# Kernel optimization log

Hardware: AMD Instinct MI355X
Metric: run time of the kernel (lower is better)

The kernel has to match this reference:

```python
import jax, jax.numpy as jnp
import numpy as np

N = 100_000   # nodes
E = 1_600_000 # edges
F = 128       # feature_dim
H = 128       # hidden_dim
C = 16        # num_classes


def setup_inputs() -> dict:
    key = jax.random.key(0)
    ks = jax.random.split(key, 7)
    x = jax.random.normal(ks[0], (N, F), dtype=jnp.float32)
    edge_index = jax.random.randint(ks[1], (2, E), 0, N, dtype=jnp.int64)
    edge_attr = jax.random.uniform(ks[2], (E,), dtype=jnp.float32)
    W1 = jax.random.normal(ks[3], (F, H), dtype=jnp.float32) / np.float32(np.sqrt(F))
    b1 = jnp.zeros((H,), jnp.float32)
    W2 = jax.random.normal(ks[4], (H, C), dtype=jnp.float32) / np.float32(np.sqrt(H))
    b2 = jnp.zeros((C,), jnp.float32)
    return {"x": x, "edge_index": edge_index, "edge_attr": edge_attr,
            "W1": W1, "b1": b1, "W2": W2, "b2": b2}


def gcn_conv(x, src, dst, ew, W, b, n):
    # PyG GCNConv: add self-loops (weight 1), symmetric degree normalization,
    # linear transform, weighted scatter-sum to destinations, bias after aggregation.
    loop = jnp.arange(n, dtype=src.dtype)
    s = jnp.concatenate([src, loop])
    d = jnp.concatenate([dst, loop])
    w = jnp.concatenate([ew, jnp.ones((n,), ew.dtype)])
    deg = jax.ops.segment_sum(w, d, num_segments=n)           # [N]
    dinv = jnp.where(deg > 0, jax.lax.rsqrt(deg), 0.0)
    norm = dinv[s] * w * dinv[d]                               # [E+N]
    h = x @ W                                                  # [N, out]
    out = jax.ops.segment_sum(h[s] * norm[:, None], d, num_segments=n)
    return out + b


def reference(x, edge_index, edge_attr, W1, b1, W2, b2):
    src, dst = edge_index[0], edge_index[1]
    h = gcn_conv(x, src, dst, edge_attr, W1, b1, N)
    h = jax.nn.relu(h)
    # dropout is identity in eval mode
    h = gcn_conv(h, src, dst, edge_attr, W2, b2, N)
    return jax.nn.softmax(h, axis=1)
```

## Files before the change

kernel.cpp:

```cpp
#include <hip/hip_runtime.h>
#include <hip/hip_fp16.h>
#include <math.h>

#define SCAN_CHUNK 2048
#define NBLK 256
#define BSH 9
#define BNODES 512


typedef __attribute__((ext_vector_type(8))) _Float16 f16x8;
typedef __attribute__((ext_vector_type(16))) float f32x16;


__global__ __launch_bounds__(256) void k_prep(const float* __restrict__ W,
                                              __half* __restrict__ W1f) {
    int tid = blockIdx.x * 256 + threadIdx.x;
    if (tid < 16384) {
        int j  = tid & 7;
        int l  = (tid >> 3) & 63;
        int ks = (tid >> 9) & 7;
        int cb = tid >> 12;
        int c = cb * 32 + (l & 31);
        int k = (l >> 5) * 8 + ks * 16 + j;
        W1f[tid] = __float2half(W[(size_t)k * 128 + c]);
    }
}


__device__ __forceinline__ void gemm1_mfma(const float* __restrict__ x,
                                           const __half* __restrict__ W1f,
                                           __half* __restrict__ h1, int n,
                                           int row0, int t, char* smem) {
    __half (*xs)[136] = (__half (*)[136])smem;
#pragma unroll
    for (int it = 0; it < 4; ++it) {
        int idx = it * 256 + t;
        int r = idx >> 5, c4 = (idx & 31) * 4;
        int gr = row0 + r;
        float4 v = (gr < n) ? *(const float4*)(x + (size_t)gr * 128 + c4)
                            : make_float4(0.f, 0.f, 0.f, 0.f);
        union { __half2 h[2]; uint2 u; } pk;
        pk.h[0] = __floats2half2_rn(v.x, v.y);
        pk.h[1] = __floats2half2_rn(v.z, v.w);
        *(uint2*)&xs[r][c4] = pk.u;
    }
    __syncthreads();

    int wv = t >> 6, lane = t & 63;
    int m = lane & 31, kh = lane >> 5;
    int col0 = wv * 32;

    f16x8 a[8], b[8];
    const __half* bp = W1f + ((size_t)wv * 8 * 64 + lane) * 8;
#pragma unroll
    for (int ks = 0; ks < 8; ++ks)
        b[ks] = *(const f16x8*)(bp + (size_t)ks * 64 * 8);
#pragma unroll
    for (int ks = 0; ks < 8; ++ks)
        a[ks] = *(const f16x8*)&xs[m][kh * 8 + ks * 16];

    f32x16 acc;
#pragma unroll
    for (int r = 0; r < 16; ++r) acc[r] = 0.f;
#pragma unroll
    for (int ks = 0; ks < 8; ++ks)
        acc = __builtin_amdgcn_mfma_f32_32x32x16_f16(a[ks], b[ks], acc, 0, 0, 0);

#pragma unroll
    for (int r = 0; r < 16; ++r) {
        int row = (r & 3) + 8 * (r >> 2) + 4 * kh;
        int g = row0 + row;
        if (g < n) h1[(size_t)g * 128 + col0 + m] = __float2half(acc[r]);
    }
}


__global__ __launch_bounds__(256) void kA(const int* __restrict__ dst, int e,
                                          int* __restrict__ hist, int nbuck,
                                          const float* __restrict__ x,
                                          const __half* __restrict__ W1f,
                                          __half* __restrict__ h1, int n,
                                          int nbB, int nbG, int gbase) {
    __shared__ char smem[32 * 136 * 2];
    int bid = blockIdx.x;
    long long T = nbB + nbG;
    long long g = ((long long)bid * nbG) / T;
    bool is_g = (((long long)(bid + 1) * nbG) / T) > g;
    int t = threadIdx.x;

    if (!is_g) {
        int* cnt = (int*)smem;
        int eb = bid - (int)g;
        for (int j = t; j < nbuck; j += 256) cnt[j] = 0;
        __syncthreads();
        long long e0 = (long long)eb * e / NBLK;
        long long e1 = (long long)(eb + 1) * e / NBLK;
        for (long long i = e0 + t; i < e1; i += 256)
            atomicAdd(&cnt[dst[i] >> BSH], 1);
        __syncthreads();
        for (int j = t; j < nbuck; j += 256)
            hist[(size_t)j * NBLK + eb] = cnt[j];
        return;
    }

    gemm1_mfma(x, W1f, h1, n, (gbase + (int)g) * 32, t, smem);
}


__global__ __launch_bounds__(256) void k_scanh(int* __restrict__ hist,
                                               int* __restrict__ bsum, int nh) {
    __shared__ int sh[256];
    int b = blockIdx.x, t = threadIdx.x;
    int base = b * SCAN_CHUNK + t * 8;
    int v[8];
    int s = 0;
#pragma unroll
    for (int j = 0; j < 8; ++j) {
        int i = base + j;
        v[j] = (i < nh) ? hist[i] : 0;
        s += v[j];
    }
    sh[t] = s;
    __syncthreads();
    for (int off = 1; off < 256; off <<= 1) {
        int u = (t >= off) ? sh[t - off] : 0;
        __syncthreads();
        sh[t] += u;
        __syncthreads();
    }
    int excl = (t > 0) ? sh[t - 1] : 0;
    if (t == 255) bsum[b] = sh[255];
    int run = excl;
#pragma unroll
    for (int j = 0; j < 8; ++j) {
        int i = base + j;
        if (i < nh) hist[i] = run;
        run += v[j];
    }
}

__global__ void k_scan2(const int* __restrict__ bsum, int* __restrict__ boff, int nb) {
    int t = threadIdx.x;
    int v = (t < nb) ? bsum[t] : 0;
    for (int off = 1; off < 64; off <<= 1) {
        int u = __shfl_up(v, off, 64);
        if (t >= off) v += u;
    }
    int e = __shfl_up(v, 1, 64);
    if (t == 0) e = 0;
    if (t < nb) boff[t] = e;
}


__global__ __launch_bounds__(256) void kB(const int* __restrict__ src,
                                          const int* __restrict__ dst,
                                          const float* __restrict__ ew, int e,
                                          const int* __restrict__ hist,
                                          const int* __restrict__ boff, int nbuck,
                                          int2* __restrict__ bucketed,
                                          const float* __restrict__ x,
                                          const __half* __restrict__ W1f,
                                          __half* __restrict__ h1, int n,
                                          int nbB, int nbG, int gbase) {
    __shared__ char smem[32 * 136 * 2];
    int bid = blockIdx.x;
    long long T = nbB + nbG;
    long long g = ((long long)bid * nbG) / T;
    bool is_g = (((long long)(bid + 1) * nbG) / T) > g;
    int t = threadIdx.x;

    if (!is_g) {
        int* wc = (int*)smem;
        int eb = bid - (int)g;
        for (int j = t; j < nbuck; j += 256) {
            int idx = j * NBLK + eb;
            wc[j] = hist[idx] + boff[idx >> 11];
        }
        __syncthreads();
        long long e0 = (long long)eb * e / NBLK;
        long long e1 = (long long)(eb + 1) * e / NBLK;
        for (long long i = e0 + t; i < e1; i += 256) {
            int d = dst[i];
            int b = d >> BSH;
            int pos = atomicAdd(&wc[b], 1);
            int2 rec;
            rec.x = src[i] | ((d & (BNODES - 1)) << 17);
            rec.y = __float_as_int(ew[i]);
            bucketed[pos] = rec;
        }
        return;
    }

    gemm1_mfma(x, W1f, h1, n, (gbase + (int)g) * 32, t, smem);
}


__global__ __launch_bounds__(256) void kC(const int2* __restrict__ bucketed,
                                          const int* __restrict__ hist,
                                          const int* __restrict__ boff,
                                          int nbuck, int n, int e,
                                          int2* __restrict__ csr,
                                          int2* __restrict__ nodeinfo,
                                          __half* __restrict__ h1) {
    __shared__ int   cnts[BNODES];
    __shared__ float degs[BNODES];
    __shared__ float dinvs[BNODES];
    __shared__ int   wcs[BNODES];
    __shared__ int   sh[256];
    int b = blockIdx.x, t = threadIdx.x;

    int i0 = b * NBLK;
    int bstart = hist[i0] + boff[i0 >> 11];
    int bend;
    if (b == nbuck - 1) bend = e;
    else {
        int i1 = (b + 1) * NBLK;
        bend = hist[i1] + boff[i1 >> 11];
    }

    cnts[t] = 0; cnts[t + 256] = 0;
    degs[t] = 0.f; degs[t + 256] = 0.f;
    __syncthreads();

    for (int i = bstart + t; i < bend; i += 256) {
        int2 rec = bucketed[i];
        int l = (rec.x >> 17) & (BNODES - 1);
        atomicAdd(&cnts[l], 1);
        atomicAdd(&degs[l], __int_as_float(rec.y));
    }
    __syncthreads();

    int c0 = cnts[2 * t], c1 = cnts[2 * t + 1];
    sh[t] = c0 + c1;
    __syncthreads();
    for (int off = 1; off < 256; off <<= 1) {
        int u = (t >= off) ? sh[t - off] : 0;
        __syncthreads();
        sh[t] += u;
        __syncthreads();
    }
    int excl = (t > 0) ? sh[t - 1] : 0;

    int rs0 = bstart + excl;
    int rs1 = rs0 + c0;
    wcs[2 * t] = rs0;
    wcs[2 * t + 1] = rs1;
#pragma unroll
    for (int q = 0; q < 2; ++q) {
        int l = 2 * t + q;
        float dv = 1.0f / sqrtf(1.0f + degs[l]);
        dinvs[l] = dv;
        int gnode = b * BNODES + l;
        if (gnode < n) {
            int2 ni;
            ni.x = (q == 0) ? rs0 : rs1;
            ni.y = __float_as_int(dv);
            nodeinfo[gnode] = ni;
        }
    }
    if (b == nbuck - 1 && t == 0) {
        int2 sent; sent.x = e; sent.y = 0;
        nodeinfo[n] = sent;
    }
    __syncthreads();

    for (int i = bstart + t; i < bend; i += 256) {
        int2 rec = bucketed[i];
        int l = (rec.x >> 17) & (BNODES - 1);
        int pos = atomicAdd(&wcs[l], 1);
        int2 o;
        o.x = rec.x & 0x1FFFF;
        o.y = rec.y;
        csr[pos] = o;
    }

    int nrows = n - b * BNODES;
    if (nrows > BNODES) nrows = BNODES;
    uint4* h1v = (uint4*)h1;
    for (int idx = t; idx < nrows * 16; idx += 256) {
        int row = idx >> 4, seg = idx & 15;
        float dv = dinvs[row];
        size_t off = ((size_t)(b * BNODES + row)) * 16 + seg;
        uint4 v = h1v[off];
        __half2* hp = (__half2*)&v;
#pragma unroll
        for (int k = 0; k < 4; ++k) {
            float2 f = __half22float2(hp[k]);
            hp[k] = __floats2half2_rn(dv * f.x, dv * f.y);
        }
        h1v[off] = v;
    }
}


__global__ __launch_bounds__(256) void k_agg1(const __half* __restrict__ h1,
                                              const int2* __restrict__ nodeinfo,
                                              const int2* __restrict__ csr,
                                              const float* __restrict__ b1,
                                              const float* __restrict__ W2g,
                                              __half* __restrict__ h2, int n) {
    __shared__ float a1s[4][128];
    __shared__ float wt[16][132];
    __shared__ float dnl[4];
    int t = threadIdx.x;
#pragma unroll
    for (int it = 0; it < 8; ++it) {
        int idx = it * 256 + t;
        wt[idx & 15][idx >> 4] = W2g[idx];
    }
    int wv = t >> 6;
    int lane = t & 63;
    int grp = lane >> 4;
    int sl = lane & 15;
    int i = blockIdx.x * 4 + wv;
    float acc[8];
#pragma unroll
    for (int k = 0; k < 8; ++k) acc[k] = 0.f;
    float di = 0.f;
    if (i < n) {
        int2 ni = nodeinfo[i];
        int begin = ni.x;
        int end = ((const int*)nodeinfo)[(size_t)(i + 1) * 2];
        di = __int_as_float(ni.y);
        if (lane == 0) dnl[wv] = di;
        if (grp == 0) {
            uint4 sv = *((const uint4*)(h1 + (size_t)i * 128) + sl);
            const __half2* hp = (const __half2*)&sv;
#pragma unroll
            for (int k = 0; k < 4; ++k) {
                float2 f = __half22float2(hp[k]);
                acc[2 * k] = f.x; acc[2 * k + 1] = f.y;
            }
        }
        int len = end - begin;
        int m = (len + 3) >> 2;
        if (m > 0) {
            int j0 = begin + grp;
            bool v0 = j0 < end;
            int2 er0 = csr[v0 ? j0 : begin];
            float w0 = v0 ? __int_as_float(er0.y) : 0.f;
            uint4 hv0 = *((const uint4*)(h1 + (size_t)er0.x * 128) + sl);
            int j1 = j0 + 4;
            bool v1 = j1 < end;
            int2 er1 = csr[v1 ? j1 : begin];
            float w1 = v1 ? __int_as_float(er1.y) : 0.f;
            for (int it2 = 1; it2 < m; ++it2) {
                uint4 hv1 = *((const uint4*)(h1 + (size_t)er1.x * 128) + sl);
                int j2 = j1 + 4;
                bool v2 = j2 < end;
                int2 er2 = csr[v2 ? j2 : begin];
                float w2 = v2 ? __int_as_float(er2.y) : 0.f;
                const __half2* hp = (const __half2*)&hv0;
#pragma unroll
                for (int k = 0; k < 4; ++k) {
                    float2 f = __half22float2(hp[k]);
                    acc[2 * k]     += w0 * f.x;
                    acc[2 * k + 1] += w0 * f.y;
                }
                hv0 = hv1; w0 = w1;
                er1 = er2; w1 = w2; j1 = j2;
            }
            const __half2* hp = (const __half2*)&hv0;
#pragma unroll
            for (int k = 0; k < 4; ++k) {
                float2 f = __half22float2(hp[k]);
                acc[2 * k]     += w0 * f.x;
                acc[2 * k + 1] += w0 * f.y;
            }
        }
    }
#pragma unroll
    for (int k = 0; k < 8; ++k) {
        acc[k] += __shfl_xor(acc[k], 16, 64);
        acc[k] += __shfl_xor(acc[k], 32, 64);
    }
    if (i < n && grp == 0) {
#pragma unroll
        for (int k = 0; k < 8; ++k)
            a1s[wv][8 * sl + k] = fmaxf(di * acc[k] + b1[8 * sl + k], 0.f);
    }
    __syncthreads();
    int oi = t >> 2, q = t & 3;
    int node = oi >> 4, c = oi & 15;
    const float* arow = a1s[node];
    float accd = 0.f;
#pragma unroll
    for (int j = 0; j < 32; ++j) accd += arow[q + 4 * j] * wt[c][q + 4 * j];
    accd += __shfl_xor(accd, 1, 64);
    accd += __shfl_xor(accd, 2, 64);
    int gi = blockIdx.x * 4 + node;
    if (q == 0 && gi < n) h2[(size_t)gi * 16 + c] = __float2half(dnl[node] * accd);
}


__global__ __launch_bounds__(256) void k_agg2(const __half* __restrict__ h2,
                                              const int2* __restrict__ nodeinfo,
                                              const int2* __restrict__ csr,
                                              const float* __restrict__ b2,
                                              float* __restrict__ out, int n) {
    int t = blockIdx.x * 256 + threadIdx.x;
    int i = t >> 4;
    int c = t & 15;
    if (i >= n) return;
    int2 ni = nodeinfo[i];
    int begin = ni.x;
    int end = ((const int*)nodeinfo)[(size_t)(i + 1) * 2];
    float di = __int_as_float(ni.y);
    float acc = __half2float(h2[(size_t)i * 16 + c]);
    int j = begin;
    for (; j + 4 <= end; j += 4) {
        int2 e0 = csr[j], e1 = csr[j + 1], e2 = csr[j + 2], e3 = csr[j + 3];
        float f0 = __half2float(h2[(size_t)e0.x * 16 + c]);
        float f1 = __half2float(h2[(size_t)e1.x * 16 + c]);
        float f2 = __half2float(h2[(size_t)e2.x * 16 + c]);
        float f3 = __half2float(h2[(size_t)e3.x * 16 + c]);
        acc += __int_as_float(e0.y) * f0;
        acc += __int_as_float(e1.y) * f1;
        acc += __int_as_float(e2.y) * f2;
        acc += __int_as_float(e3.y) * f3;
    }
    for (; j < end; ++j) {
        int2 e0 = csr[j];
        acc += __int_as_float(e0.y) * __half2float(h2[(size_t)e0.x * 16 + c]);
    }
    acc = di * acc + b2[c];
    float m = acc;
    for (int off = 8; off; off >>= 1) m = fmaxf(m, __shfl_xor(m, off, 16));
    float ex = expf(acc - m);
    float ssum = ex;
    for (int off = 8; off; off >>= 1) ssum += __shfl_xor(ssum, off, 16);
    out[(size_t)i * 16 + c] = ex / ssum;
}


extern "C" void kernel_launch(void* const* d_in, const int* in_sizes, int n_in,
                              void* d_out, int out_size, void* d_ws, size_t ws_size,
                              hipStream_t stream) {
    const float* x  = (const float*)d_in[0];
    const int*   ei = (const int*)d_in[1];
    const float* ew = (const float*)d_in[2];
    const float* W1 = (const float*)d_in[3];
    const float* b1 = (const float*)d_in[4];
    const float* W2 = (const float*)d_in[5];
    const float* b2 = (const float*)d_in[6];
    float* out = (float*)d_out;

    const int N = in_sizes[0] / 128;
    const int E = in_sizes[2];
    const int* src = ei;
    const int* dst = ei + E;

    const int nbuck = (N + BNODES - 1) >> BSH;
    const int nh = nbuck * NBLK;
    const int nbS = (nh + SCAN_CHUNK - 1) / SCAN_CHUNK;

    char* w = (char*)d_ws;
    int2*   bucketed = (int2*)w;              w += (size_t)E * 8;
    int2*   csr      = (int2*)w;              w += (size_t)E * 8;
    __half* h1       = (__half*)w;            w += (size_t)N * 128 * 2;
    __half* h2       = (__half*)w;            w += (size_t)N * 16 * 2;
    int2*   nodeinfo = (int2*)w;              w += (size_t)(N + 2) * 8;
    int*    hist     = (int*)w;               w += (size_t)nh * 4;
    int*    bsum     = (int*)w;               w += 64 * 4;
    int*    boff     = (int*)w;               w += 64 * 4;
    __half* W1f      = (__half*)w;            w += (size_t)16384 * 2;

    int nbG_total = (N + 31) / 32;
    int nbG1 = nbG_total / 2;
    int nbG2 = nbG_total - nbG1;

    k_prep<<<64, 256, 0, stream>>>(W1, W1f);
    kA<<<NBLK + nbG1, 256, 0, stream>>>(dst, E, hist, nbuck, x, W1f, h1, N,
                                        NBLK, nbG1, 0);
    k_scanh<<<nbS, 256, 0, stream>>>(hist, bsum, nh);
    k_scan2<<<1, 64, 0, stream>>>(bsum, boff, nbS);
    kB<<<NBLK + nbG2, 256, 0, stream>>>(src, dst, ew, E, hist, boff, nbuck,
                                        bucketed, x, W1f, h1, N, NBLK, nbG2, nbG1);
    kC<<<nbuck, 256, 0, stream>>>(bucketed, hist, boff, nbuck, N, E,
                                  csr, nodeinfo, h1);
    k_agg1<<<(N + 3) / 4, 256, 0, stream>>>(h1, nodeinfo, csr, b1, W2, h2, N);
    k_agg2<<<(N + 15) / 16, 256, 0, stream>>>(h2, nodeinfo, csr, b2, out, N);
}
```

Before: 218.5 us.

## Fold scan2 into consumers, move dinv scaling into aggregation, overlap GEMM with kC

Removes the single-block k_scan2 launch by having each consumer block scan the block sums itself in shared memory. Drops the in-place dinv rescaling pass over h1 in kC and instead multiplies the source node's dinv into each edge weight inside k_agg1, and scales the self term by di. This frees kC so a third share of the GEMM blocks can run alongside it. Edge loads in kA and kB are vectorised to int4, with slice boundaries aligned to multiples of 4. The cost is an extra gathered nodeinfo read per edge in aggregation, plus a slightly less even GEMM split across three kernels.

Measured after the change: 196.7 us. -10.0%, faster.

```diff
diff --git a/kernel.cpp b/kernel.cpp
--- a/kernel.cpp
+++ b/kernel.cpp
@@ -72,6 +72,10 @@
         int g = row0 + row;
         if (g < n) h1[(size_t)g * 128 + col0 + m] = __float2half(acc[r]);
     }
+}
+
+__device__ __forceinline__ long long sl_begin(int eb, int e) {
+    return ((long long)eb * e / NBLK) & ~3LL;
 }
 
 
@@ -93,9 +97,17 @@
         int eb = bid - (int)g;
         for (int j = t; j < nbuck; j += 256) cnt[j] = 0;
         __syncthreads();
-        long long e0 = (long long)eb * e / NBLK;
-        long long e1 = (long long)(eb + 1) * e / NBLK;
-        for (long long i = e0 + t; i < e1; i += 256)
+        long long e0 = sl_begin(eb, e);
+        long long e1 = (eb == NBLK - 1) ? e : sl_begin(eb + 1, e);
+        for (long long i = e0 + (long long)t * 4; i + 3 < e1; i += 1024) {
+            int4 d4 = *(const int4*)(dst + i);
+            atomicAdd(&cnt[d4.x >> BSH], 1);
+            atomicAdd(&cnt[d4.y >> BSH], 1);
+            atomicAdd(&cnt[d4.z >> BSH], 1);
+            atomicAdd(&cnt[d4.w >> BSH], 1);
+        }
+        long long vend = e0 + ((e1 - e0) & ~3LL);
+        for (long long i = vend + t; i < e1; i += 256)
             atomicAdd(&cnt[dst[i] >> BSH], 1);
         __syncthreads();
         for (int j = t; j < nbuck; j += 256)
@@ -139,16 +151,17 @@
     }
 }
 
-__global__ void k_scan2(const int* __restrict__ bsum, int* __restrict__ boff, int nb) {
-    int t = threadIdx.x;
-    int v = (t < nb) ? bsum[t] : 0;
-    for (int off = 1; off < 64; off <<= 1) {
-        int u = __shfl_up(v, off, 64);
-        if (t >= off) v += u;
-    }
-    int e = __shfl_up(v, 1, 64);
-    if (t == 0) e = 0;
-    if (t < nb) boff[t] = e;
+__device__ __forceinline__ void scan_bsum(const int* __restrict__ bsum, int nbS,
+                                          int* boffs, int t) {
+    if (t < 32) {
+        int raw = (t < nbS) ? bsum[t] : 0;
+        int v = raw;
+        for (int off = 1; off < 32; off <<= 1) {
+            int u = __shfl_up(v, off, 64);
+            if (t >= off) v += u;
+        }
+        boffs[t] = v - raw;
+    }
 }
 
 
@@ -156,7 +169,8 @@
                                           const int* __restrict__ dst,
                                           const float* __restrict__ ew, int e,
                                           const int* __restrict__ hist,
-                                          const int* __restrict__ boff, int nbuck,
+                                          const int* __restrict__ bsum, int nbS,
+                                          int nbuck,
                                           int2* __restrict__ bucketed,
                                           const float* __restrict__ x,
                                           const __half* __restrict__ W1f,
@@ -171,15 +185,42 @@
 
     if (!is_g) {
         int* wc = (int*)smem;
+        int* boffs = (int*)(smem + 2048);
         int eb = bid - (int)g;
+        scan_bsum(bsum, nbS, boffs, t);
+        __syncthreads();
         for (int j = t; j < nbuck; j += 256) {
             int idx = j * NBLK + eb;
-            wc[j] = hist[idx] + boff[idx >> 11];
-        }
-        __syncthreads();
-        long long e0 = (long long)eb * e / NBLK;
-        long long e1 = (long long)(eb + 1) * e / NBLK;
-        for (long long i = e0 + t; i < e1; i += 256) {
+            wc[j] = hist[idx] + boffs[idx >> 11];
+        }
+        __syncthreads();
+        long long e0 = sl_begin(eb, e);
+        long long e1 = (eb == NBLK - 1) ? e : sl_begin(eb + 1, e);
+        for (long long i = e0 + (long long)t * 4; i + 3 < e1; i += 1024) {
+            int4 d4 = *(const int4*)(dst + i);
+            int4 s4 = *(const int4*)(src + i);
+            float4 w4 = *(const float4*)(ew + i);
+            int2 rec;
+            int pos;
+            pos = atomicAdd(&wc[d4.x >> BSH], 1);
+            rec.x = s4.x | ((d4.x & (BNODES - 1)) << 17);
+            rec.y = __float_as_int(w4.x);
+            bucketed[pos] = rec;
+            pos = atomicAdd(&wc[d4.y >> BSH], 1);
+            rec.x = s4.y | ((d4.y & (BNODES - 1)) << 17);
+            rec.y = __float_as_int(w4.y);
+            bucketed[pos] = rec;
+            pos = atomicAdd(&wc[d4.z >> BSH], 1);
+            rec.x = s4.z | ((d4.z & (BNODES - 1)) << 17);
+            rec.y = __float_as_int(w4.z);
+            bucketed[pos] = rec;
+            pos = atomicAdd(&wc[d4.w >> BSH], 1);
+            rec.x = s4.w | ((d4.w & (BNODES - 1)) << 17);
+            rec.y = __float_as_int(w4.w);
+            bucketed[pos] = rec;
+        }
+        long long vend = e0 + ((e1 - e0) & ~3LL);
+        for (long long i = vend + t; i < e1; i += 256) {
             int d = dst[i];
             int b = d >> BSH;
             int pos = atomicAdd(&wc[b], 1);
@@ -197,30 +238,41 @@
 
 __global__ __launch_bounds__(256) void kC(const int2* __restrict__ bucketed,
                                           const int* __restrict__ hist,
-                                          const int* __restrict__ boff,
+                                          const int* __restrict__ bsum, int nbS,
                                           int nbuck, int n, int e,
                                           int2* __restrict__ csr,
                                           int2* __restrict__ nodeinfo,
-                                          __half* __restrict__ h1) {
-    __shared__ int   cnts[BNODES];
-    __shared__ float degs[BNODES];
-    __shared__ float dinvs[BNODES];
-    __shared__ int   wcs[BNODES];
-    __shared__ int   sh[256];
-    int b = blockIdx.x, t = threadIdx.x;
+                                          const float* __restrict__ x,
+                                          const __half* __restrict__ W1f,
+                                          __half* __restrict__ h1, int gbase) {
+    __shared__ char smem[32 * 136 * 2];
+    int bid = blockIdx.x, t = threadIdx.x;
+
+    if (bid >= nbuck) {
+        gemm1_mfma(x, W1f, h1, n, (gbase + bid - nbuck) * 32, t, smem);
+        return;
+    }
+
+    int*   cnts  = (int*)smem;
+    float* degs  = (float*)(smem + 2048);
+    int*   wcs   = (int*)(smem + 4096);
+    int*   sh    = (int*)(smem + 6144);
+    int*   boffs = (int*)(smem + 7168);
+    int b = bid;
+
+    scan_bsum(bsum, nbS, boffs, t);
+    cnts[t] = 0; cnts[t + 256] = 0;
+    degs[t] = 0.f; degs[t + 256] = 0.f;
+    __syncthreads();
 
     int i0 = b * NBLK;
-    int bstart = hist[i0] + boff[i0 >> 11];
+    int bstart = hist[i0] + boffs[i0 >> 11];
     int bend;
     if (b == nbuck - 1) bend = e;
     else {
         int i1 = (b + 1) * NBLK;
-        bend = hist[i1] + boff[i1 >> 11];
-    }
-
-    cnts[t] = 0; cnts[t + 256] = 0;
-    degs[t] = 0.f; degs[t + 256] = 0.f;
-    __syncthreads();
+        bend = hist[i1] + boffs[i1 >> 11];
+    }
 
     for (int i = bstart + t; i < bend; i += 256) {
         int2 rec = bucketed[i];
@@ -249,7 +301,6 @@
     for (int q = 0; q < 2; ++q) {
         int l = 2 * t + q;
         float dv = 1.0f / sqrtf(1.0f + degs[l]);
-        dinvs[l] = dv;
         int gnode = b * BNODES + l;
         if (gnode < n) {
             int2 ni;
@@ -272,23 +323,6 @@
         o.x = rec.x & 0x1FFFF;
         o.y = rec.y;
         csr[pos] = o;
-    }
-
-    int nrows = n - b * BNODES;
-    if (nrows > BNODES) nrows = BNODES;
-    uint4* h1v = (uint4*)h1;
-    for (int idx = t; idx < nrows * 16; idx += 256) {
-        int row = idx >> 4, seg = idx & 15;
-        float dv = dinvs[row];
-        size_t off = ((size_t)(b * BNODES + row)) * 16 + seg;
-        uint4 v = h1v[off];
-        __half2* hp = (__half2*)&v;
-#pragma unroll
-        for (int k = 0; k < 4; ++k) {
-            float2 f = __half22float2(hp[k]);
-            hp[k] = __floats2half2_rn(dv * f.x, dv * f.y);
-        }
-        h1v[off] = v;
     }
 }
 
@@ -313,6 +347,7 @@
     int grp = lane >> 4;
     int sl = lane & 15;
     int i = blockIdx.x * 4 + wv;
+    const int* nis = (const int*)nodeinfo;
     float acc[8];
 #pragma unroll
     for (int k = 0; k < 8; ++k) acc[k] = 0.f;
@@ -320,7 +355,7 @@
     if (i < n) {
         int2 ni = nodeinfo[i];
         int begin = ni.x;
-        int end = ((const int*)nodeinfo)[(size_t)(i + 1) * 2];
+        int end = nis[(size_t)(i + 1) * 2];
         di = __int_as_float(ni.y);
         if (lane == 0) dnl[wv] = di;
         if (grp == 0) {
@@ -329,7 +364,7 @@
 #pragma unroll
             for (int k = 0; k < 4; ++k) {
                 float2 f = __half22float2(hp[k]);
-                acc[2 * k] = f.x; acc[2 * k + 1] = f.y;
+                acc[2 * k] = di * f.x; acc[2 * k + 1] = di * f.y;
             }
         }
         int len = end - begin;
@@ -338,18 +373,21 @@
             int j0 = begin + grp;
             bool v0 = j0 < end;
             int2 er0 = csr[v0 ? j0 : begin];
-            float w0 = v0 ? __int_as_float(er0.y) : 0.f;
+            float w0 = v0 ? __int_as_float(er0.y) *
+                            __int_as_float(nis[2 * (size_t)er0.x + 1]) : 0.f;
             uint4 hv0 = *((const uint4*)(h1 + (size_t)er0.x * 128) + sl);
             int j1 = j0 + 4;
             bool v1 = j1 < end;
             int2 er1 = csr[v1 ? j1 : begin];
-            float w1 = v1 ? __int_as_float(er1.y) : 0.f;
+            float w1 = v1 ? __int_as_float(er1.y) *
+                            __int_as_float(nis[2 * (size_t)er1.x + 1]) : 0.f;
             for (int it2 = 1; it2 < m; ++it2) {
                 uint4 hv1 = *((const uint4*)(h1 + (size_t)er1.x * 128) + sl);
                 int j2 = j1 + 4;
                 bool v2 = j2 < end;
                 int2 er2 = csr[v2 ? j2 : begin];
-                float w2 = v2 ? __int_as_float(er2.y) : 0.f;
+                float w2 = v2 ? __int_as_float(er2.y) *
+                                __int_as_float(nis[2 * (size_t)er2.x + 1]) : 0.f;
                 const __half2* hp = (const __half2*)&hv0;
 #pragma unroll
                 for (int k = 0; k < 4; ++k) {
@@ -462,22 +500,21 @@
     int2*   nodeinfo = (int2*)w;              w += (size_t)(N + 2) * 8;
     int*    hist     = (int*)w;               w += (size_t)nh * 4;
     int*    bsum     = (int*)w;               w += 64 * 4;
-    int*    boff     = (int*)w;               w += 64 * 4;
     __half* W1f      = (__half*)w;            w += (size_t)16384 * 2;
 
     int nbG_total = (N + 31) / 32;
-    int nbG1 = nbG_total / 2;
-    int nbG2 = nbG_total - nbG1;
+    int nbG3 = 625;
+    int nbG1 = (nbG_total - nbG3) / 2;
+    int nbG2 = nbG_total - nbG3 - nbG1;
 
     k_prep<<<64, 256, 0, stream>>>(W1, W1f);
     kA<<<NBLK + nbG1, 256, 0, stream>>>(dst, E, hist, nbuck, x, W1f, h1, N,
                                         NBLK, nbG1, 0);
     k_scanh<<<nbS, 256, 0, stream>>>(hist, bsum, nh);
-    k_scan2<<<1, 64, 0, stream>>>(bsum, boff, nbS);
-    kB<<<NBLK + nbG2, 256, 0, stream>>>(src, dst, ew, E, hist, boff, nbuck,
+    kB<<<NBLK + nbG2, 256, 0, stream>>>(src, dst, ew, E, hist, bsum, nbS, nbuck,
                                         bucketed, x, W1f, h1, N, NBLK, nbG2, nbG1);
-    kC<<<nbuck, 256, 0, stream>>>(bucketed, hist, boff, nbuck, N, E,
-                                  csr, nodeinfo, h1);
+    kC<<<nbuck + nbG3, 256, 0, stream>>>(bucketed, hist, bsum, nbS, nbuck, N, E,
+                                         csr, nodeinfo, x, W1f, h1, nbG1 + nbG2);
     k_agg1<<<(N + 3) / 4, 256, 0, stream>>>(h1, nodeinfo, csr, b1, W2, h2, N);
     k_agg2<<<(N + 15) / 16, 256, 0, stream>>>(h2, nodeinfo, csr, b2, out, N);
 }
```
